# Performance work log

Measured on AMD Instinct MI355X. Metric: run time of the kernel, lower is better.

## Reference

```python
import jax, jax.numpy as jnp
import numpy as np

LEAKY = 0.2     # PyG GATConv leaky_relu negative slope
BN_EPS = 1e-5

N, E, F_IN = 100000, 1600000, 7
ENC, HID, HEADS = 64, 32, 4
HC = HID * HEADS          # 128
DEC_IN, OUT = 64, 4
N_HIDDEN = 2              # nb_hidden_layers - 1


def gat_conv(z, src, dst, W, a_src, a_dst, b, concat):
    # PyG GATConv (shared lin for src/dst), dropout in eval mode = identity.
    n = z.shape[0]
    H, C = a_src.shape
    h = (z @ W).reshape(n, H, C)                      # [N,H,C]
    al_s = jnp.einsum('nhc,hc->nh', h, a_src)         # [N,H]
    al_d = jnp.einsum('nhc,hc->nh', h, a_dst)
    e = jax.nn.leaky_relu(al_s[src] + al_d[dst], LEAKY)   # [E,H]
    m = jax.ops.segment_max(e, dst, num_segments=n)       # scatter-softmax over in-edges
    ex = jnp.exp(e - m[dst])
    denom = jax.ops.segment_sum(ex, dst, num_segments=n)
    alpha = ex / (denom[dst] + 1e-16)                     # [E,H]
    out = jax.ops.segment_sum(h[src] * alpha[:, :, None], dst, num_segments=n)  # [N,H,C]
    out = out.reshape(n, H * C) if concat else out.mean(axis=1)
    return out + b


def batch_norm(z, gamma, beta):
    # track_running_stats=False -> always use batch statistics (biased var)
    mu = z.mean(axis=0)
    var = z.var(axis=0)
    return gamma * (z - mu) * jax.lax.rsqrt(var + BN_EPS) + beta


def setup_inputs() -> dict:
    key = jax.random.key(0)
    ks = jax.random.split(key, 20)
    g = lambda k, shape, fan: jax.random.normal(k, shape, jnp.float32) * (1.0 / np.sqrt(fan))
    inp = {
        'x': jax.random.normal(ks[0], (N, F_IN), jnp.float32),
        'edge_index': jax.random.randint(ks[1], (2, E), 0, N, jnp.int32),
        'enc_W': g(ks[2], (F_IN, ENC), F_IN),
        'enc_b': jnp.zeros((ENC,), jnp.float32),
        'in_W': g(ks[3], (ENC, HC), ENC),
        'in_att_src': g(ks[4], (HEADS, HID), HID),
        'in_att_dst': g(ks[5], (HEADS, HID), HID),
        'in_b': jnp.zeros((HC,), jnp.float32),
        'hid_W': g(ks[6], (N_HIDDEN, HC, HC), HC),
        'hid_att_src': g(ks[7], (N_HIDDEN, HEADS, HID), HID),
        'hid_att_dst': g(ks[8], (N_HIDDEN, HEADS, HID), HID),
        'hid_b': jnp.zeros((N_HIDDEN, HC), jnp.float32),
        'bn_gamma': jnp.ones((1 + N_HIDDEN, HC), jnp.float32),
        'bn_beta': jnp.zeros((1 + N_HIDDEN, HC), jnp.float32),
        'out_W': g(ks[9], (HC, DEC_IN), HC),           # out heads=1, concat=False
        'out_att_src': g(ks[10], (1, DEC_IN), DEC_IN),
        'out_att_dst': g(ks[11], (1, DEC_IN), DEC_IN),
        'out_b': jnp.zeros((DEC_IN,), jnp.float32),
        'dec_W': g(ks[12], (DEC_IN, OUT), DEC_IN),
        'dec_b': jnp.zeros((OUT,), jnp.float32),
    }
    return inp


def reference(x, edge_index, enc_W, enc_b, in_W, in_att_src, in_att_dst, in_b,
              hid_W, hid_att_src, hid_att_dst, hid_b, bn_gamma, bn_beta,
              out_W, out_att_src, out_att_dst, out_b, dec_W, dec_b):
    n = x.shape[0]
    loops = jnp.arange(n, dtype=edge_index.dtype)      # PyG GATConv add_self_loops=True
    src = jnp.concatenate([edge_index[0], loops])
    dst = jnp.concatenate([edge_index[1], loops])

    z = x @ enc_W + enc_b                              # encoder
    z = gat_conv(z, src, dst, in_W, in_att_src, in_att_dst, in_b, concat=True)
    z = jax.nn.relu(batch_norm(z, bn_gamma[0], bn_beta[0]))
    for i in range(N_HIDDEN):
        z = gat_conv(z, src, dst, hid_W[i], hid_att_src[i], hid_att_dst[i], hid_b[i], concat=True)
        z = jax.nn.relu(batch_norm(z, bn_gamma[i + 1], bn_beta[i + 1]))
    z = gat_conv(z, src, dst, out_W, out_att_src, out_att_dst, out_b, concat=False)
    z = z @ dec_W + dec_b                              # decoder
    return z
```

## Files before the change

kernel.cpp:

```cpp
#include <hip/hip_runtime.h>
#include <math.h>

#define LEAKY 0.2f
#define BN_EPS 1e-5f

typedef unsigned short u16;
typedef __bf16 bf16x8 __attribute__((ext_vector_type(8)));
typedef float f32x4 __attribute__((ext_vector_type(4)));
typedef u16 ushort8 __attribute__((ext_vector_type(8)));

__device__ __forceinline__ u16 f2bf(float x){
    unsigned u = __float_as_uint(x);
    u += 0x7FFFu + ((u >> 16) & 1u);
    return (u16)(u >> 16);
}
__device__ __forceinline__ float bf2f(u16 b){ return __uint_as_float(((unsigned)b) << 16); }


__global__ __launch_bounds__(256) void k_encoder(const float* __restrict__ x,
        const float* __restrict__ W, const float* __restrict__ b,
        float* __restrict__ z, int N){
    int gid = blockIdx.x*256 + threadIdx.x;
    int n = gid >> 6, j = gid & 63;
    if (n >= N) return;
    float acc = b[j];
    #pragma unroll
    for (int k=0;k<7;k++) acc += x[n*7+k]*W[k*64+j];
    z[(size_t)n*64+j] = acc;
}

template<int K, int M>
__global__ __launch_bounds__(256) void k_pack_w(const float* __restrict__ W,
        u16* __restrict__ hi, u16* __restrict__ lo){
    int idx = blockIdx.x*256 + threadIdx.x;
    if (idx >= K*M) return;
    int e = idx & 7, l16 = (idx >> 3) & 3, rest = idx >> 5;
    int n = rest % M, t = rest / M;
    int k = t*32 + l16*8 + e;
    float w = W[(size_t)k*M + n];
    u16 hb = f2bf(w);
    hi[idx] = hb;
    lo[idx] = f2bf(w - bf2f(hb));
}

__global__ void k_bn_coef(const float* __restrict__ cs, const float* __restrict__ cq,
        const float* __restrict__ g, const float* __restrict__ be,
        float* __restrict__ scale, float* __restrict__ shift, float invN){
    int j = threadIdx.x;
    float mu = cs[j]*invN;
    float var = cq[j]*invN - mu*mu;
    float s = g[j]*rsqrtf(var + BN_EPS);
    scale[j] = s; shift[j] = be[j] - mu*s;
}


template<int H>
__global__ __launch_bounds__(256) void k_mh1(const float* __restrict__ al,
        float* __restrict__ pm, int total){
    int t = threadIdx.x;
    float m = -1e30f;
    for (int i = blockIdx.x*256 + t; i < total; i += 64*256)
        m = fmaxf(m, al[i]);
    #pragma unroll
    for (int off = H; off < 64; off <<= 1)
        m = fmaxf(m, __shfl_xor(m, off, 64));
    __shared__ float ws[16];
    int lane = t & 63, wid = t >> 6;
    if (lane < H) ws[wid*H + lane] = m;
    __syncthreads();
    if (t < H){
        float mm = ws[t];
        #pragma unroll
        for (int w = 1; w < 4; w++) mm = fmaxf(mm, ws[w*H + t]);
        pm[blockIdx.x*H + t] = mm;
    }
}

template<int H>
__global__ void k_mh2(const float* __restrict__ pm, float* __restrict__ mh){
    int t = threadIdx.x;
    float m = -1e30f;
    #pragma unroll
    for (int k = 0; k < H; k++) m = fmaxf(m, pm[t + k*64]);
    #pragma unroll
    for (int off = H; off < 64; off <<= 1)
        m = fmaxf(m, __shfl_xor(m, off, 64));
    if (t < H) mh[t] = m;
}

template<int K, int M, int RW, int CW, int WR, int WC, int H, bool BNIN>
__global__ __launch_bounds__(256) void k_gemm(const float* __restrict__ z,
        const u16* __restrict__ Whi, const u16* __restrict__ Wlo,
        const float* __restrict__ bnscale, const float* __restrict__ bnshift,
        const float* __restrict__ a_src, const float* __restrict__ a_dst,
        u16* __restrict__ hout, float* __restrict__ al_s, float* __restrict__ al_d,
        int N)
{
    static_assert(RW*CW == 4 && RW*WR*16 == 64 && CW*WC*16 == M, "tile config");
    constexpr int KS = K/32;
    constexpr int KG = K/8;
    __shared__ __align__(16) u16 Ahi[64*K];
    __shared__ __align__(16) u16 Alo[64*K];
    const int brow = blockIdx.x*64;
    const int tid = threadIdx.x;

    for (int u = tid; u < 64*KG; u += 256){
        int row = u / KG, kg = u % KG;
        int gr = brow + row;
        float v[8];
        if (gr < N){
            const float4* p = (const float4*)(z + (size_t)gr*K + kg*8);
            float4 a = p[0], bq = p[1];
            v[0]=a.x; v[1]=a.y; v[2]=a.z; v[3]=a.w;
            v[4]=bq.x; v[5]=bq.y; v[6]=bq.z; v[7]=bq.w;
            if (BNIN){
                const float4* sc = (const float4*)(bnscale + kg*8);
                const float4* sh = (const float4*)(bnshift + kg*8);
                float4 s0=sc[0], s1=sc[1], t0=sh[0], t1=sh[1];
                v[0]=fmaxf(fmaf(v[0],s0.x,t0.x),0.f);
                v[1]=fmaxf(fmaf(v[1],s0.y,t0.y),0.f);
                v[2]=fmaxf(fmaf(v[2],s0.z,t0.z),0.f);
                v[3]=fmaxf(fmaf(v[3],s0.w,t0.w),0.f);
                v[4]=fmaxf(fmaf(v[4],s1.x,t1.x),0.f);
                v[5]=fmaxf(fmaf(v[5],s1.y,t1.y),0.f);
                v[6]=fmaxf(fmaf(v[6],s1.z,t1.z),0.f);
                v[7]=fmaxf(fmaf(v[7],s1.w,t1.w),0.f);
            }
        } else {
            #pragma unroll
            for (int e=0;e<8;e++) v[e]=0.f;
        }
        ushort8 h8, l8;
        #pragma unroll
        for (int e=0;e<8;e++){
            u16 hb = f2bf(v[e]);
            h8[e] = hb;
            l8[e] = f2bf(v[e] - bf2f(hb));
        }
        int rb = row >> 4, t = kg >> 2, lg = kg & 3;
        int base = (((rb*KS + t)*64) + (row & 15) + 16*lg)*8;
        *(ushort8*)&Ahi[base] = h8;
        *(ushort8*)&Alo[base] = l8;
    }
    __syncthreads();

    const int wave = tid >> 6, lane = tid & 63;
    const int wrow = wave / CW, wcol = wave % CW;
    const int l15 = lane & 15, l16 = lane >> 4;

    f32x4 acc[WR][WC];
    #pragma unroll
    for (int r=0;r<WR;r++)
        #pragma unroll
        for (int c=0;c<WC;c++) acc[r][c] = (f32x4){0.f,0.f,0.f,0.f};

    #pragma unroll
    for (int t = 0; t < KS; ++t){
        bf16x8 ah[WR], al[WR];
        #pragma unroll
        for (int r=0;r<WR;r++){
            int rb = wrow*WR + r;
            int off = ((rb*KS + t)*64 + lane)*8;
            ah[r] = *(const bf16x8*)&Ahi[off];
            al[r] = *(const bf16x8*)&Alo[off];
        }
        bf16x8 bh[WC], bl[WC];
        #pragma unroll
        for (int c=0;c<WC;c++){
            int n = (wcol*WC + c)*16 + l15;
            size_t off = ((size_t)(t*M + n)*4 + (size_t)l16)*8;
            bh[c] = *(const bf16x8*)&Whi[off];
            bl[c] = *(const bf16x8*)&Wlo[off];
        }
        #pragma unroll
        for (int r=0;r<WR;r++)
            #pragma unroll
            for (int c=0;c<WC;c++){
                acc[r][c] = __builtin_amdgcn_mfma_f32_16x16x32_bf16(al[r], bh[c], acc[r][c], 0,0,0);
                acc[r][c] = __builtin_amdgcn_mfma_f32_16x16x32_bf16(ah[r], bl[c], acc[r][c], 0,0,0);
                acc[r][c] = __builtin_amdgcn_mfma_f32_16x16x32_bf16(ah[r], bh[c], acc[r][c], 0,0,0);
            }
    }

    float as_[WC], ad_[WC];
    #pragma unroll
    for (int c=0;c<WC;c++){
        int colg = (wcol*WC + c)*16 + l15;
        as_[c] = a_src[colg]; ad_[c] = a_dst[colg];
    }
    #pragma unroll
    for (int r=0;r<WR;r++){
        #pragma unroll
        for (int q=0;q<4;q++){
            int rowg = brow + (wrow*WR + r)*16 + l16*4 + q;
            float s0=0.f,d0=0.f,s1=0.f,d1=0.f;
            #pragma unroll
            for (int c=0;c<WC;c++){
                float av = acc[r][c][q];
                if (H==1 || c < WC/2){ s0 += av*as_[c]; d0 += av*ad_[c]; }
                else                 { s1 += av*as_[c]; d1 += av*ad_[c]; }
            }
            #pragma unroll
            for (int off=1; off<16; off<<=1){
                s0 += __shfl_xor(s0, off, 64); d0 += __shfl_xor(d0, off, 64);
                if (H==4){ s1 += __shfl_xor(s1, off, 64); d1 += __shfl_xor(d1, off, 64); }
            }
            if (l15 == 0 && rowg < N){
                if (H==4){
                    al_s[(size_t)rowg*4 + wcol*2]     = s0;
                    al_s[(size_t)rowg*4 + wcol*2 + 1] = s1;
                    al_d[(size_t)rowg*4 + wcol*2]     = d0;
                    al_d[(size_t)rowg*4 + wcol*2 + 1] = d1;
                } else {
                    al_s[rowg] = s0; al_d[rowg] = d0;
                }
            }
        }
    }

    #pragma unroll
    for (int r=0;r<WR;r++)
        #pragma unroll
        for (int c=0;c<WC;c++){
            int colg = (wcol*WC + c)*16 + l15;
            #pragma unroll
            for (int q=0;q<4;q++){
                int rowg = brow + (wrow*WR + r)*16 + l16*4 + q;
                if (rowg < N) hout[(size_t)rowg*M + colg] = f2bf(acc[r][c][q]);
            }
        }
}


__global__ __launch_bounds__(256) void k_deg(const int* __restrict__ ei, int E,
        int* __restrict__ deg){
    int e = blockIdx.x*256 + threadIdx.x;
    if (e < E) atomicAdd(deg + ei[E+e], 1);
}

__device__ __forceinline__ int wave_scan(int v, int lane){
    #pragma unroll
    for (int off=1; off<64; off<<=1){
        int t = __shfl_up(v, off, 64);
        if (lane >= off) v += t;
    }
    return v;
}

__global__ __launch_bounds__(1024) void k_scan1(const int* __restrict__ deg,
        int* __restrict__ excl, int* __restrict__ bsum, int N){
    __shared__ int ws[16];
    int i = blockIdx.x*1024 + threadIdx.x;
    int lane = threadIdx.x & 63, wid = threadIdx.x >> 6;
    int v = (i < N) ? deg[i] : 0;
    int inc = wave_scan(v, lane);
    if (lane == 63) ws[wid] = inc;
    __syncthreads();
    if (wid == 0){
        int wv = (lane < 16) ? ws[lane] : 0;
        int winc = wave_scan(wv, lane);
        if (lane < 16) ws[lane] = winc - wv;
    }
    __syncthreads();
    int off = ws[wid];
    if (i < N) excl[i] = off + inc - v;
    if (threadIdx.x == 1023) bsum[blockIdx.x] = off + inc;
}

__global__ void k_scan2(int* __restrict__ bsum, int nb){
    if (threadIdx.x == 0 && blockIdx.x == 0){
        int c = 0;
        for (int i = 0; i < nb; i++){ int t = bsum[i]; bsum[i] = c; c += t; }
    }
}

__global__ __launch_bounds__(256) void k_scan3(const int* __restrict__ excl,
        const int* __restrict__ bsum, int* __restrict__ rowptr,
        int* __restrict__ cursor, int N, int E){
    int i = blockIdx.x*256 + threadIdx.x;
    if (i < N){
        int r = excl[i] + bsum[i >> 10];
        rowptr[i] = r; cursor[i] = r;
    } else if (i == N){
        rowptr[N] = E;
    }
}

__global__ __launch_bounds__(256) void k_bucket(const int* __restrict__ ei, int E,
        int* __restrict__ cursor, int* __restrict__ csr){
    int e = blockIdx.x*256 + threadIdx.x;
    if (e >= E) return;
    int pos = atomicAdd(cursor + ei[E+e], 1);
    csr[pos] = ei[e];
}


template<int H, int C, bool STATS, bool DECODE>
__global__ __launch_bounds__(256) void k_gat_agg(
        const int* __restrict__ rowptr, const int* __restrict__ csr_src,
        const float* __restrict__ al_s, const float* __restrict__ al_d,
        const float* __restrict__ mh,
        const u16* __restrict__ hfeat, const float* __restrict__ b,
        float* __restrict__ z, float* __restrict__ cs, float* __restrict__ cq,
        const float* __restrict__ decW, const float* __restrict__ decb,
        float* __restrict__ out, int N, int totWaves)
{
    constexpr int M = H*C;
    constexpr int EL = M/64;
    const int lane = threadIdx.x & 63;
    const int j = EL*lane;
    const int h = j / C;
    const int gw = blockIdx.x*4 + (threadIdx.x >> 6);

    const float bj0 = b[j];
    const float bj1 = (EL==2) ? b[j+1] : 0.f;
    const float mhf = mh[h];
    float w0=0,w1=0,w2=0,w3=0;
    if (DECODE){ w0=decW[lane*4]; w1=decW[lane*4+1]; w2=decW[lane*4+2]; w3=decW[lane*4+3]; }
    float ls0=0.f, ls1=0.f, lq0=0.f, lq1=0.f;

    for (int dst = gw; dst < N; dst += totWaves){
        int p0 = rowptr[dst], p1 = rowptr[dst+1];
        float ald = al_d[(size_t)dst*H + h];
        float t = mhf + ald;
        float mb = t > 0.f ? t : LEAKY*t;
        float v0 = al_s[(size_t)dst*H + h] + ald;
        v0 = v0 > 0.f ? v0 : LEAKY*v0;
        mb = fminf(mb, v0 + 40.f);

        float ex0 = __expf(v0 - mb);
        float s = ex0;
        float acc0, acc1 = 0.f;
        if (EL==2){
            unsigned hv = *(const unsigned*)(hfeat + (size_t)dst*M + j);
            acc0 = bf2f((u16)hv)*ex0; acc1 = bf2f((u16)(hv>>16))*ex0;
        } else {
            acc0 = bf2f(hfeat[(size_t)dst*M + j])*ex0;
        }

        auto ld = [&](int idx, unsigned& hv, float& vs){
            if (idx < p1){
                int src = csr_src[idx];
                vs = al_s[(size_t)src*H + h];
                if (EL==2) hv = *(const unsigned*)(hfeat + (size_t)src*M + j);
                else       hv = (unsigned)hfeat[(size_t)src*M + j];
            }
        };
        auto proc = [&](unsigned hv, float vs){
            float vv = vs + ald;
            vv = vv > 0.f ? vv : LEAKY*vv;
            float ex = __expf(vv - mb);
            s += ex;
            acc0 = fmaf(bf2f((u16)hv), ex, acc0);
            if (EL==2) acc1 = fmaf(bf2f((u16)(hv>>16)), ex, acc1);
        };

        unsigned hA0=0,hA1=0,hA2=0,hA3=0, hB0=0,hB1=0,hB2=0,hB3=0;
        float vA0=0,vA1=0,vA2=0,vA3=0, vB0=0,vB1=0,vB2=0,vB3=0;
        int p = p0;
        ld(p, hA0, vA0); ld(p+1, hA1, vA1); ld(p+2, hA2, vA2); ld(p+3, hA3, vA3);
        while (p < p1){
            ld(p+4, hB0, vB0); ld(p+5, hB1, vB1); ld(p+6, hB2, vB2); ld(p+7, hB3, vB3);
            proc(hA0, vA0);
            if (p+1 < p1) proc(hA1, vA1);
            if (p+2 < p1) proc(hA2, vA2);
            if (p+3 < p1) proc(hA3, vA3);
            p += 4;
            if (p >= p1) break;
            ld(p+4, hA0, vA0); ld(p+5, hA1, vA1); ld(p+6, hA2, vA2); ld(p+7, hA3, vA3);
            proc(hB0, vB0);
            if (p+1 < p1) proc(hB1, vB1);
            if (p+2 < p1) proc(hB2, vB2);
            if (p+3 < p1) proc(hB3, vB3);
            p += 4;
        }

        float inv = 1.f/s;
        float o0 = acc0*inv + bj0;
        float o1 = (EL==2) ? acc1*inv + bj1 : 0.f;
        if (STATS){ ls0+=o0; lq0+=o0*o0; ls1+=o1; lq1+=o1*o1; }
        if (!DECODE){
            if (EL==2) *(float2*)(z + (size_t)dst*M + j) = make_float2(o0,o1);
            else       z[(size_t)dst*M + j] = o0;
        } else {
            float a0=o0*w0, a1=o0*w1, a2=o0*w2, a3=o0*w3;
            #pragma unroll
            for (int off=32; off; off>>=1){
                a0 += __shfl_xor(a0, off, 64);
                a1 += __shfl_xor(a1, off, 64);
                a2 += __shfl_xor(a2, off, 64);
                a3 += __shfl_xor(a3, off, 64);
            }
            if (lane == 0){
                float4 o = make_float4(a0+decb[0], a1+decb[1], a2+decb[2], a3+decb[3]);
                *(float4*)(out + (size_t)dst*4) = o;
            }
        }
    }
    if (STATS){
        __shared__ float sls[128], slq[128];
        if (threadIdx.x < 128){ sls[threadIdx.x]=0.f; slq[threadIdx.x]=0.f; }
        __syncthreads();
        atomicAdd(&sls[j], ls0);  atomicAdd(&slq[j], lq0);
        if (EL==2){ atomicAdd(&sls[j+1], ls1); atomicAdd(&slq[j+1], lq1); }
        __syncthreads();
        if (threadIdx.x < 128){
            atomicAdd(cs + threadIdx.x, sls[threadIdx.x]);
            atomicAdd(cq + threadIdx.x, slq[threadIdx.x]);
        }
    }
}

extern "C" void kernel_launch(void* const* d_in, const int* in_sizes, int n_in,
                              void* d_out, int out_size, void* d_ws, size_t ws_size,
                              hipStream_t stream){
    const float* x      = (const float*)d_in[0];
    const int*   ei     = (const int*)  d_in[1];
    const float* enc_W  = (const float*)d_in[2];
    const float* enc_b  = (const float*)d_in[3];
    const float* in_W   = (const float*)d_in[4];
    const float* in_as  = (const float*)d_in[5];
    const float* in_ad  = (const float*)d_in[6];
    const float* in_b   = (const float*)d_in[7];
    const float* hid_W  = (const float*)d_in[8];
    const float* hid_as = (const float*)d_in[9];
    const float* hid_ad = (const float*)d_in[10];
    const float* hid_b  = (const float*)d_in[11];
    const float* bn_g   = (const float*)d_in[12];
    const float* bn_b   = (const float*)d_in[13];
    const float* out_W  = (const float*)d_in[14];
    const float* out_as = (const float*)d_in[15];
    const float* out_ad = (const float*)d_in[16];
    const float* out_b  = (const float*)d_in[17];
    const float* dec_W  = (const float*)d_in[18];
    const float* dec_b  = (const float*)d_in[19];

    const int N = in_sizes[0] / 7;
    const int E = in_sizes[1] / 2;
    const int NB = (N + 1023) / 1024;
    const int NT = (N + 63) / 64;
    const int AGG_BLOCKS = 2048, TOT_WAVES = AGG_BLOCKS*4;

    float*    bufZ   = (float*)d_ws;
    float*    al_s   = bufZ + (size_t)N*128;
    float*    al_d   = al_s + (size_t)N*4;
    float*    cs     = al_d + (size_t)N*4;
    float*    cq     = cs + 128;
    float*    mh     = cq + 128;
    float*    pm     = mh + 8;
    float*    scale  = pm + 256;
    float*    shift  = scale + 128;
    int*      deg    = (int*)(shift + 128);
    int*      excl   = deg + N;
    int*      rowptr = excl + N;
    int*      cursor = rowptr + (N+1);
    int*      bsum   = cursor + N;
    int*      csr    = bsum + NB;
    u16*      hb     = (u16*)(((uintptr_t)(csr + E) + 15) & ~(uintptr_t)15);
    u16*      wk     = hb + (size_t)N*128;
    u16* wk_in_hi  = wk;                    u16* wk_in_lo  = wk_in_hi  + 64*128;
    u16* wk_h0_hi  = wk_in_lo  + 64*128;    u16* wk_h0_lo  = wk_h0_hi  + 128*128;
    u16* wk_h1_hi  = wk_h0_lo  + 128*128;   u16* wk_h1_lo  = wk_h1_hi  + 128*128;
    u16* wk_out_hi = wk_h1_lo  + 128*128;   u16* wk_out_lo = wk_out_hi + 128*64;

    k_pack_w<64,128><<<(64*128+255)/256, 256, 0, stream>>>(in_W, wk_in_hi, wk_in_lo);
    k_pack_w<128,128><<<(128*128+255)/256, 256, 0, stream>>>(hid_W, wk_h0_hi, wk_h0_lo);
    k_pack_w<128,128><<<(128*128+255)/256, 256, 0, stream>>>(hid_W + 128*128, wk_h1_hi, wk_h1_lo);
    k_pack_w<128,64><<<(128*64+255)/256, 256, 0, stream>>>(out_W, wk_out_hi, wk_out_lo);

    hipMemsetAsync(deg, 0, (size_t)N*sizeof(int), stream);
    k_deg   <<<(E+255)/256, 256, 0, stream>>>(ei, E, deg);
    k_scan1 <<<NB, 1024, 0, stream>>>(deg, excl, bsum, N);
    k_scan2 <<<1, 64, 0, stream>>>(bsum, NB);
    k_scan3 <<<(N+1+255)/256, 256, 0, stream>>>(excl, bsum, rowptr, cursor, N, E);
    k_bucket<<<(E+255)/256, 256, 0, stream>>>(ei, E, cursor, csr);

    k_encoder<<<(N*64+255)/256, 256, 0, stream>>>(x, enc_W, enc_b, bufZ, N);

    const float invN = 1.f/(float)N;

    hipMemsetAsync(cs, 0, 256*sizeof(float), stream);
    k_gemm<64,128,2,2,2,4,4,false><<<NT, 256, 0, stream>>>(bufZ, wk_in_hi, wk_in_lo,
            nullptr, nullptr, in_as, in_ad, hb, al_s, al_d, N);
    k_mh1<4><<<64, 256, 0, stream>>>(al_s, pm, N*4);
    k_mh2<4><<<1, 64, 0, stream>>>(pm, mh);
    k_gat_agg<4,32,true,false><<<AGG_BLOCKS, 256, 0, stream>>>(rowptr, csr, al_s, al_d, mh,
            hb, in_b, bufZ, cs, cq, nullptr, nullptr, nullptr, N, TOT_WAVES);
    k_bn_coef<<<1, 128, 0, stream>>>(cs, cq, bn_g, bn_b, scale, shift, invN);

    for (int i = 0; i < 2; i++){
        const u16* whi = i ? wk_h1_hi : wk_h0_hi;
        const u16* wlo = i ? wk_h1_lo : wk_h0_lo;
        hipMemsetAsync(cs, 0, 256*sizeof(float), stream);
        k_gemm<128,128,2,2,2,4,4,true><<<NT, 256, 0, stream>>>(bufZ, whi, wlo,
                scale, shift, hid_as + (size_t)i*128, hid_ad + (size_t)i*128,
                hb, al_s, al_d, N);
        k_mh1<4><<<64, 256, 0, stream>>>(al_s, pm, N*4);
        k_mh2<4><<<1, 64, 0, stream>>>(pm, mh);
        k_gat_agg<4,32,true,false><<<AGG_BLOCKS, 256, 0, stream>>>(rowptr, csr, al_s, al_d, mh,
                hb, hid_b + (size_t)i*128, bufZ, cs, cq, nullptr, nullptr, nullptr, N, TOT_WAVES);
        k_bn_coef<<<1, 128, 0, stream>>>(cs, cq, bn_g + (i+1)*128, bn_b + (i+1)*128, scale, shift, invN);
    }

    k_gemm<128,64,4,1,1,4,1,true><<<NT, 256, 0, stream>>>(bufZ, wk_out_hi, wk_out_lo,
            scale, shift, out_as, out_ad, hb, al_s, al_d, N);
    k_mh1<1><<<64, 256, 0, stream>>>(al_s, pm, N);
    k_mh2<1><<<1, 64, 0, stream>>>(pm, mh);
    k_gat_agg<1,64,false,true><<<AGG_BLOCKS, 256, 0, stream>>>(rowptr, csr, al_s, al_d, mh,
            hb, out_b, nullptr, nullptr, nullptr, dec_W, dec_b, (float*)d_out, N, TOT_WAVES);
}
```

Baseline: 979.3 us.

## Process multiple edges per wave with 16-byte feature loads in GAT aggregation

```diff
diff --git a/kernel.cpp b/kernel.cpp
--- a/kernel.cpp
+++ b/kernel.cpp
@@ -306,103 +306,131 @@
         float* __restrict__ out, int N, int totWaves)
 {
     constexpr int M = H*C;
-    constexpr int EL = M/64;
+    constexpr int GS = M/8;
+    constexpr int EPS = 64/GS;
     const int lane = threadIdx.x & 63;
-    const int j = EL*lane;
-    const int h = j / C;
+    const int q = lane % GS;
+    const int g = lane / GS;
+    const int col0 = q*8;
+    const int hd = col0 / C;
     const int gw = blockIdx.x*4 + (threadIdx.x >> 6);
 
-    const float bj0 = b[j];
-    const float bj1 = (EL==2) ? b[j+1] : 0.f;
-    const float mhf = mh[h];
-    float w0=0,w1=0,w2=0,w3=0;
-    if (DECODE){ w0=decW[lane*4]; w1=decW[lane*4+1]; w2=decW[lane*4+2]; w3=decW[lane*4+3]; }
-    float ls0=0.f, ls1=0.f, lq0=0.f, lq1=0.f;
+    const float mhf = mh[hd];
+    float bj[8];
+    #pragma unroll
+    for (int j=0;j<8;j++) bj[j] = b[col0+j];
+
+    float w[8][4];
+    if (DECODE){
+        #pragma unroll
+        for (int j=0;j<8;j++)
+            #pragma unroll
+            for (int o=0;o<4;o++) w[j][o] = decW[(col0+j)*4 + o];
+    }
+    float ls[8], lq[8];
+    if (STATS){
+        #pragma unroll
+        for (int j=0;j<8;j++){ ls[j]=0.f; lq[j]=0.f; }
+    }
 
     for (int dst = gw; dst < N; dst += totWaves){
         int p0 = rowptr[dst], p1 = rowptr[dst+1];
-        float ald = al_d[(size_t)dst*H + h];
-        float t = mhf + ald;
-        float mb = t > 0.f ? t : LEAKY*t;
-        float v0 = al_s[(size_t)dst*H + h] + ald;
+        float ald = al_d[(size_t)dst*H + hd];
+        float v0 = al_s[(size_t)dst*H + hd] + ald;
         v0 = v0 > 0.f ? v0 : LEAKY*v0;
+        float tt = mhf + ald;
+        float mb = tt > 0.f ? tt : LEAKY*tt;
         mb = fminf(mb, v0 + 40.f);
 
-        float ex0 = __expf(v0 - mb);
+        float ex0 = __expf(v0 - mb) * (1.0f/EPS);
         float s = ex0;
-        float acc0, acc1 = 0.f;
-        if (EL==2){
-            unsigned hv = *(const unsigned*)(hfeat + (size_t)dst*M + j);
-            acc0 = bf2f((u16)hv)*ex0; acc1 = bf2f((u16)(hv>>16))*ex0;
-        } else {
-            acc0 = bf2f(hfeat[(size_t)dst*M + j])*ex0;
-        }
-
-        auto ld = [&](int idx, unsigned& hv, float& vs){
-            if (idx < p1){
-                int src = csr_src[idx];
-                vs = al_s[(size_t)src*H + h];
-                if (EL==2) hv = *(const unsigned*)(hfeat + (size_t)src*M + j);
-                else       hv = (unsigned)hfeat[(size_t)src*M + j];
-            }
+        float acc[8];
+        ushort8 hd8 = *(const ushort8*)(hfeat + (size_t)dst*M + col0);
+        #pragma unroll
+        for (int j=0;j<8;j++) acc[j] = bf2f(hd8[j]) * ex0;
+
+        auto LD = [&](int base, ushort8& hv, float& vs){
+            int idx = base + g;
+            int src = dst;
+            if (idx < p1) src = csr_src[idx];
+            float t = al_s[(size_t)src*H + hd];
+            vs = (idx < p1) ? t : -1e30f;
+            hv = *(const ushort8*)(hfeat + (size_t)src*M + col0);
         };
-        auto proc = [&](unsigned hv, float vs){
+        auto PR = [&](const ushort8& hv, float vs){
             float vv = vs + ald;
             vv = vv > 0.f ? vv : LEAKY*vv;
             float ex = __expf(vv - mb);
             s += ex;
-            acc0 = fmaf(bf2f((u16)hv), ex, acc0);
-            if (EL==2) acc1 = fmaf(bf2f((u16)(hv>>16)), ex, acc1);
+            #pragma unroll
+            for (int j=0;j<8;j++) acc[j] = fmaf(bf2f(hv[j]), ex, acc[j]);
         };
 
-        unsigned hA0=0,hA1=0,hA2=0,hA3=0, hB0=0,hB1=0,hB2=0,hB3=0;
-        float vA0=0,vA1=0,vA2=0,vA3=0, vB0=0,vB1=0,vB2=0,vB3=0;
+        ushort8 hvA, hvB; float vsA=0.f, vsB=0.f;
         int p = p0;
-        ld(p, hA0, vA0); ld(p+1, hA1, vA1); ld(p+2, hA2, vA2); ld(p+3, hA3, vA3);
+        LD(p, hvA, vsA);
         while (p < p1){
-            ld(p+4, hB0, vB0); ld(p+5, hB1, vB1); ld(p+6, hB2, vB2); ld(p+7, hB3, vB3);
-            proc(hA0, vA0);
-            if (p+1 < p1) proc(hA1, vA1);
-            if (p+2 < p1) proc(hA2, vA2);
-            if (p+3 < p1) proc(hA3, vA3);
-            p += 4;
+            LD(p+EPS, hvB, vsB);
+            PR(hvA, vsA);
+            p += EPS;
             if (p >= p1) break;
-            ld(p+4, hA0, vA0); ld(p+5, hA1, vA1); ld(p+6, hA2, vA2); ld(p+7, hA3, vA3);
-            proc(hB0, vB0);
-            if (p+1 < p1) proc(hB1, vB1);
-            if (p+2 < p1) proc(hB2, vB2);
-            if (p+3 < p1) proc(hB3, vB3);
-            p += 4;
-        }
-
+            LD(p+EPS, hvA, vsA);
+            PR(hvB, vsB);
+            p += EPS;
+        }
+
+        #pragma unroll
+        for (int off = GS; off < 64; off <<= 1){
+            s += __shfl_xor(s, off, 64);
+            #pragma unroll
+            for (int j=0;j<8;j++) acc[j] += __shfl_xor(acc[j], off, 64);
+        }
         float inv = 1.f/s;
-        float o0 = acc0*inv + bj0;
-        float o1 = (EL==2) ? acc1*inv + bj1 : 0.f;
-        if (STATS){ ls0+=o0; lq0+=o0*o0; ls1+=o1; lq1+=o1*o1; }
+        float o8[8];
+        #pragma unroll
+        for (int j=0;j<8;j++) o8[j] = acc[j]*inv + bj[j];
+
+        if (STATS){
+            #pragma unroll
+            for (int j=0;j<8;j++){ ls[j] += o8[j]; lq[j] += o8[j]*o8[j]; }
+        }
         if (!DECODE){
-            if (EL==2) *(float2*)(z + (size_t)dst*M + j) = make_float2(o0,o1);
-            else       z[(size_t)dst*M + j] = o0;
+            if (lane < GS){
+                float4 w0 = make_float4(o8[0],o8[1],o8[2],o8[3]);
+                float4 w1 = make_float4(o8[4],o8[5],o8[6],o8[7]);
+                *(float4*)(z + (size_t)dst*M + col0)     = w0;
+                *(float4*)(z + (size_t)dst*M + col0 + 4) = w1;
+            }
         } else {
-            float a0=o0*w0, a1=o0*w1, a2=o0*w2, a3=o0*w3;
-            #pragma unroll
-            for (int off=32; off; off>>=1){
-                a0 += __shfl_xor(a0, off, 64);
-                a1 += __shfl_xor(a1, off, 64);
-                a2 += __shfl_xor(a2, off, 64);
-                a3 += __shfl_xor(a3, off, 64);
+            float p4[4] = {0.f,0.f,0.f,0.f};
+            #pragma unroll
+            for (int j=0;j<8;j++)
+                #pragma unroll
+                for (int o=0;o<4;o++) p4[o] = fmaf(o8[j], w[j][o], p4[o]);
+            #pragma unroll
+            for (int off=1; off<GS; off<<=1){
+                #pragma unroll
+                for (int o=0;o<4;o++) p4[o] += __shfl_xor(p4[o], off, 64);
             }
             if (lane == 0){
-                float4 o = make_float4(a0+decb[0], a1+decb[1], a2+decb[2], a3+decb[3]);
+                float4 o = make_float4(p4[0]+decb[0], p4[1]+decb[1],
+                                       p4[2]+decb[2], p4[3]+decb[3]);
                 *(float4*)(out + (size_t)dst*4) = o;
             }
         }
     }
+
     if (STATS){
         __shared__ float sls[128], slq[128];
         if (threadIdx.x < 128){ sls[threadIdx.x]=0.f; slq[threadIdx.x]=0.f; }
         __syncthreads();
-        atomicAdd(&sls[j], ls0);  atomicAdd(&slq[j], lq0);
-        if (EL==2){ atomicAdd(&sls[j+1], ls1); atomicAdd(&slq[j+1], lq1); }
+        if (lane < GS){
+            #pragma unroll
+            for (int j=0;j<8;j++){
+                atomicAdd(&sls[col0+j], ls[j]);
+                atomicAdd(&slq[col0+j], lq[j]);
+            }
+        }
         __syncthreads();
         if (threadIdx.x < 128){
             atomicAdd(cs + threadIdx.x, sls[threadIdx.x]);
```

Measured after the change: 925.5 us. 1.06x faster.
